# Kernel optimization log

Hardware: AMD Instinct MI355X
Metric: run time of the kernel (lower is better)

The kernel has to match this reference:

```python
import jax, jax.numpy as jnp
import numpy as np

N_HEADS = 16
DIMS = 1024
HEAD_SIZE = DIMS // N_HEADS


def setup_inputs() -> dict:
    key = jax.random.key(0)
    k1, k2, k3, k4, k5 = jax.random.split(key, 5)
    x = jax.random.normal(k1, (1, 4096, DIMS), dtype=jnp.float32)
    s = 1.0 / np.sqrt(DIMS)
    w_qkv = jax.random.uniform(k2, (3 * DIMS, DIMS), jnp.float32, -s, s)
    b_qkv = jax.random.uniform(k3, (3 * DIMS,), jnp.float32, -s, s)
    w_o = jax.random.uniform(k4, (DIMS, DIMS), jnp.float32, -s, s)
    b_o = jax.random.uniform(k5, (DIMS,), jnp.float32, -s, s)
    return {"x": x, "w_qkv": w_qkv, "b_qkv": b_qkv, "w_o": w_o, "b_o": b_o,
            "causal_mask": 1}


def reference(x, w_qkv, b_qkv, w_o, b_o, causal_mask):
    B, S, D = x.shape
    qkv = x @ w_qkv.T + b_qkv                      # [B,S,3D]
    q, k, v = jnp.split(qkv, 3, axis=-1)
    def heads(t):
        return t.reshape(B, S, N_HEADS, HEAD_SIZE).transpose(0, 2, 1, 3)  # [B,H,S,hd]
    q, k, v = heads(q), heads(k), heads(v)
    scores = jnp.einsum("bhsd,bhtd->bhst", q, k)   # [B,H,S,S]
    if causal_mask:
        tri = jnp.triu(jnp.ones((S, S), dtype=bool), k=1)
        scores = jnp.where(tri, -jnp.inf, scores)  # mask BEFORE scale, as in torch code
    scores = scores / np.sqrt(HEAD_SIZE)
    weights = jax.nn.softmax(scores, axis=-1)
    out = jnp.einsum("bhst,bhtd->bhsd", weights, v)  # [B,H,S,hd]
    out = out.transpose(0, 2, 1, 3).reshape(B, S, D)
    return out @ w_o.T + b_o
```

## Files before the change

kernel.cpp:

```cpp
#include <hip/hip_runtime.h>
#include <hip/hip_bf16.h>
#include <stdint.h>

typedef __attribute__((ext_vector_type(8))) short short8;
typedef __attribute__((ext_vector_type(4))) float f32x4;
typedef __attribute__((ext_vector_type(16))) float f32x16;
typedef __attribute__((ext_vector_type(2))) unsigned int uint2u;
typedef __hip_bfloat16 bf16;

#define S_LEN 4096
#define DMODEL 1024
#define NH 16
#define HD 64
#define QSCALE 0.1803368801111f

static __device__ inline uint2 pack4(float4 v) {
  union { uint2 u; bf16 h[4]; } p;
  p.h[0] = (bf16)v.x; p.h[1] = (bf16)v.y; p.h[2] = (bf16)v.z; p.h[3] = (bf16)v.w;
  return p.u;
}

static __device__ inline uint32_t pack2(float a, float b) {
  union { uint32_t u; bf16 h[2]; } p;
  p.h[0] = (bf16)a; p.h[1] = (bf16)b;
  return p.u;
}

static __device__ inline void gload_lds16(const bf16* g, bf16* l) {
  __builtin_amdgcn_global_load_lds(
      (const __attribute__((address_space(1))) unsigned int*)g,
      (__attribute__((address_space(3))) unsigned int*)l, 16, 0, 0);
}

static __device__ inline int rot_idx(int r, int c) {
  return r * 64 + ((c + ((r & 7) << 3)) & 63);
}

__global__ __launch_bounds__(256)
void cvt_all(const float* __restrict__ x, const float* __restrict__ wq,
             const float* __restrict__ wo, bf16* __restrict__ xb,
             bf16* __restrict__ wqb, bf16* __restrict__ wob) {
  const int nx = S_LEN * DMODEL;
  const int nq = 3 * DMODEL * DMODEL;
  const int no = DMODEL * DMODEL;
  int i = (blockIdx.x * 256 + threadIdx.x) * 4;
  if (i < nx) {
    *(uint2*)(xb + i) = pack4(*(const float4*)(x + i));
  } else if (i < nx + nq) {
    int j = i - nx;
    *(uint2*)(wqb + j) = pack4(*(const float4*)(wq + j));
  } else if (i < nx + nq + no) {
    int j = i - nx - nq;
    *(uint2*)(wob + j) = pack4(*(const float4*)(wo + j));
  }
}

__global__ __launch_bounds__(256)
void gemm_qkv(const bf16* __restrict__ A, const bf16* __restrict__ B,
              const float* __restrict__ bias, bf16* __restrict__ qkv2,
              bf16* __restrict__ vt) {
  const int K = DMODEL;
  __shared__ bf16 sA[128 * 64];
  __shared__ bf16 sB[128 * 64];
  const int tid  = threadIdx.x;
  const int lane = tid & 63;
  const int wave = tid >> 6;
  const int wm = wave >> 1, wn = wave & 1;
  const int tileM = blockIdx.y * 128;
  const int tileN = blockIdx.x * 128;

  const int lrow = lane & 15;
  const int quad = lane >> 4;
  const int kq   = quad * 8;

  f32x4 acc[4][4];
#pragma unroll
  for (int i = 0; i < 4; i++)
#pragma unroll
    for (int j = 0; j < 4; j++) acc[i][j] = (f32x4){0.f, 0.f, 0.f, 0.f};

  const int trl = lane >> 3;
  const int cgl = (((lane & 7) - trl) & 7) << 3;
  const bf16* aP[4];
  const bf16* bP[4];
#pragma unroll
  for (int c = 0; c < 4; c++) {
    int ch = wave * 4 + c;
    aP[c] = A + (size_t)(tileM + ch * 8 + trl) * K + cgl;
    bP[c] = B + (size_t)(tileN + ch * 8 + trl) * K + cgl;
  }

  for (int k0 = 0; k0 < K; k0 += 64) {
    __syncthreads();
#pragma unroll
    for (int c = 0; c < 4; c++) {
      int ch = wave * 4 + c;
      gload_lds16(aP[c] + k0, sA + ch * 512);
      gload_lds16(bP[c] + k0, sB + ch * 512);
    }
    __syncthreads();
#pragma unroll
    for (int ks = 0; ks < 2; ks++) {
      short8 afrag[4], bfrag[4];
#pragma unroll
      for (int mi = 0; mi < 4; mi++)
        afrag[mi] = *(const short8*)(sA + rot_idx(wm * 64 + mi * 16 + lrow, ks * 32 + kq));
#pragma unroll
      for (int ni = 0; ni < 4; ni++)
        bfrag[ni] = *(const short8*)(sB + rot_idx(wn * 64 + ni * 16 + lrow, ks * 32 + kq));
#pragma unroll
      for (int mi = 0; mi < 4; mi++)
#pragma unroll
        for (int ni = 0; ni < 4; ni++)
          acc[mi][ni] = __builtin_amdgcn_mfma_f32_16x16x32_bf16(afrag[mi], bfrag[ni], acc[mi][ni], 0, 0, 0);
    }
  }

#pragma unroll
  for (int ni = 0; ni < 4; ni++) {
    int col = tileN + wn * 64 + ni * 16 + lrow;
    float bv = bias[col];
    if (col < 2 * DMODEL) {
      float sc = (col < DMODEL) ? QSCALE : 1.0f;
#pragma unroll
      for (int mi = 0; mi < 4; mi++) {
        int row0 = tileM + wm * 64 + mi * 16 + quad * 4;
#pragma unroll
        for (int r = 0; r < 4; r++)
          qkv2[(size_t)(row0 + r) * 2048 + col] = (bf16)((acc[mi][ni][r] + bv) * sc);
      }
    } else {
      int cc = col - 2 * DMODEL;
      int hh = cc >> 6, dd = cc & 63;
      bf16* vrow = vt + ((size_t)(hh * 64 + dd)) * S_LEN;
#pragma unroll
      for (int mi = 0; mi < 4; mi++) {
        int row0 = tileM + wm * 64 + mi * 16 + quad * 4;
        float4 v = {acc[mi][ni][0] + bv, acc[mi][ni][1] + bv,
                    acc[mi][ni][2] + bv, acc[mi][ni][3] + bv};
        *(uint2*)(vrow + row0) = pack4(v);
      }
    }
  }
}

__global__ __launch_bounds__(256)
void gemm_oproj(const bf16* __restrict__ A, const bf16* __restrict__ B,
                const float* __restrict__ bias, float* __restrict__ C) {
  const int K = DMODEL, N = DMODEL;
  __shared__ bf16 sA[128 * 64];
  __shared__ bf16 sB[64 * 64];
  const int tid  = threadIdx.x;
  const int lane = tid & 63;
  const int wave = tid >> 6;
  const int wm = wave >> 1, wn = wave & 1;
  const int tileM = blockIdx.y * 128;
  const int tileN = blockIdx.x * 64;

  const int lrow = lane & 15;
  const int quad = lane >> 4;
  const int kq   = quad * 8;

  f32x4 acc[4][2];
#pragma unroll
  for (int i = 0; i < 4; i++)
#pragma unroll
    for (int j = 0; j < 2; j++) acc[i][j] = (f32x4){0.f, 0.f, 0.f, 0.f};

  const int trl = lane >> 3;
  const int cgl = (((lane & 7) - trl) & 7) << 3;
  const bf16* aP[4];
  const bf16* bP[2];
#pragma unroll
  for (int c = 0; c < 4; c++) {
    int ch = wave * 4 + c;
    aP[c] = A + (size_t)(tileM + ch * 8 + trl) * K + cgl;
  }
#pragma unroll
  for (int c = 0; c < 2; c++) {
    int ch = wave * 2 + c;
    bP[c] = B + (size_t)(tileN + ch * 8 + trl) * K + cgl;
  }

  for (int k0 = 0; k0 < K; k0 += 64) {
    __syncthreads();
#pragma unroll
    for (int c = 0; c < 4; c++)
      gload_lds16(aP[c] + k0, sA + (wave * 4 + c) * 512);
#pragma unroll
    for (int c = 0; c < 2; c++)
      gload_lds16(bP[c] + k0, sB + (wave * 2 + c) * 512);
    __syncthreads();
#pragma unroll
    for (int ks = 0; ks < 2; ks++) {
      short8 afrag[4], bfrag[2];
#pragma unroll
      for (int mi = 0; mi < 4; mi++)
        afrag[mi] = *(const short8*)(sA + rot_idx(wm * 64 + mi * 16 + lrow, ks * 32 + kq));
#pragma unroll
      for (int ni = 0; ni < 2; ni++)
        bfrag[ni] = *(const short8*)(sB + rot_idx(wn * 32 + ni * 16 + lrow, ks * 32 + kq));
#pragma unroll
      for (int mi = 0; mi < 4; mi++)
#pragma unroll
        for (int ni = 0; ni < 2; ni++)
          acc[mi][ni] = __builtin_amdgcn_mfma_f32_16x16x32_bf16(afrag[mi], bfrag[ni], acc[mi][ni], 0, 0, 0);
    }
  }

#pragma unroll
  for (int ni = 0; ni < 2; ni++) {
    int col = tileN + wn * 32 + ni * 16 + lrow;
    float bv = bias[col];
#pragma unroll
    for (int mi = 0; mi < 4; mi++) {
      int row0 = tileM + wm * 64 + mi * 16 + quad * 4;
#pragma unroll
      for (int r = 0; r < 4; r++)
        C[(size_t)(row0 + r) * N + col] = acc[mi][ni][r] + bv;
    }
  }
}

__global__ __launch_bounds__(256)
void gemm_qkv_f32(const float* __restrict__ A, const float* __restrict__ B,
                  const float* __restrict__ bias, bf16* __restrict__ qkv2,
                  bf16* __restrict__ vt) {
  const int K = DMODEL;
  __shared__ bf16 sA[128 * 64];
  __shared__ bf16 sB[128 * 64];
  const int tid  = threadIdx.x;
  const int lane = tid & 63;
  const int wave = tid >> 6;
  const int wm = wave >> 1, wn = wave & 1;
  const int tileM = blockIdx.y * 128;
  const int tileN = blockIdx.x * 128;
  const int lrow = lane & 15;
  const int quad = lane >> 4;
  const int kq   = quad * 8;

  f32x4 acc[4][4];
#pragma unroll
  for (int i = 0; i < 4; i++)
#pragma unroll
    for (int j = 0; j < 4; j++) acc[i][j] = (f32x4){0.f, 0.f, 0.f, 0.f};

  const int r0 = tid >> 4;
  const int cc = (tid & 15) * 4;

  for (int k0 = 0; k0 < K; k0 += 64) {
    uint2 ra[8], rb[8];
#pragma unroll
    for (int i = 0; i < 8; i++) {
      int row = r0 + i * 16;
      ra[i] = pack4(*(const float4*)(A + (size_t)(tileM + row) * K + k0 + cc));
      rb[i] = pack4(*(const float4*)(B + (size_t)(tileN + row) * K + k0 + cc));
    }
    __syncthreads();
#pragma unroll
    for (int i = 0; i < 8; i++) {
      int row = r0 + i * 16;
      *(uint2*)(sA + row * 64 + cc) = ra[i];
      *(uint2*)(sB + row * 64 + cc) = rb[i];
    }
    __syncthreads();
#pragma unroll
    for (int ks = 0; ks < 2; ks++) {
      short8 afrag[4], bfrag[4];
#pragma unroll
      for (int mi = 0; mi < 4; mi++)
        afrag[mi] = *(const short8*)(sA + (wm * 64 + mi * 16 + lrow) * 64 + ks * 32 + kq);
#pragma unroll
      for (int ni = 0; ni < 4; ni++)
        bfrag[ni] = *(const short8*)(sB + (wn * 64 + ni * 16 + lrow) * 64 + ks * 32 + kq);
#pragma unroll
      for (int mi = 0; mi < 4; mi++)
#pragma unroll
        for (int ni = 0; ni < 4; ni++)
          acc[mi][ni] = __builtin_amdgcn_mfma_f32_16x16x32_bf16(afrag[mi], bfrag[ni], acc[mi][ni], 0, 0, 0);
    }
  }
#pragma unroll
  for (int ni = 0; ni < 4; ni++) {
    int col = tileN + wn * 64 + ni * 16 + lrow;
    float bv = bias[col];
    if (col < 2 * DMODEL) {
      float sc = (col < DMODEL) ? QSCALE : 1.0f;
#pragma unroll
      for (int mi = 0; mi < 4; mi++) {
        int row0 = tileM + wm * 64 + mi * 16 + quad * 4;
#pragma unroll
        for (int r = 0; r < 4; r++)
          qkv2[(size_t)(row0 + r) * 2048 + col] = (bf16)((acc[mi][ni][r] + bv) * sc);
      }
    } else {
      int c2 = col - 2 * DMODEL;
      int hh = c2 >> 6, dd = c2 & 63;
      bf16* vrow = vt + ((size_t)(hh * 64 + dd)) * S_LEN;
#pragma unroll
      for (int mi = 0; mi < 4; mi++) {
        int row0 = tileM + wm * 64 + mi * 16 + quad * 4;
        float4 v = {acc[mi][ni][0] + bv, acc[mi][ni][1] + bv,
                    acc[mi][ni][2] + bv, acc[mi][ni][3] + bv};
        *(uint2*)(vrow + row0) = pack4(v);
      }
    }
  }
}

__global__ __launch_bounds__(256)
void gemm_oproj_f32w(const bf16* __restrict__ A, const float* __restrict__ B,
                     const float* __restrict__ bias, float* __restrict__ C) {
  const int K = DMODEL, N = DMODEL;
  __shared__ bf16 sA[128 * 64];
  __shared__ bf16 sB[128 * 64];
  const int tid  = threadIdx.x;
  const int lane = tid & 63;
  const int wave = tid >> 6;
  const int wm = wave >> 1, wn = wave & 1;
  const int tileM = blockIdx.y * 128;
  const int tileN = blockIdx.x * 128;
  const int lrow = lane & 15;
  const int quad = lane >> 4;
  const int kq   = quad * 8;

  f32x4 acc[4][4];
#pragma unroll
  for (int i = 0; i < 4; i++)
#pragma unroll
    for (int j = 0; j < 4; j++) acc[i][j] = (f32x4){0.f, 0.f, 0.f, 0.f};

  const int a_r0 = tid >> 3;
  const int a_cc = (tid & 7) * 8;
  const int b_r0 = tid >> 4;
  const int b_cc = (tid & 15) * 4;

  for (int k0 = 0; k0 < K; k0 += 64) {
    uint4 ra[4];
    uint2 rb[8];
#pragma unroll
    for (int i = 0; i < 4; i++)
      ra[i] = *(const uint4*)(A + (size_t)(tileM + a_r0 + i * 32) * K + k0 + a_cc);
#pragma unroll
    for (int i = 0; i < 8; i++)
      rb[i] = pack4(*(const float4*)(B + (size_t)(tileN + b_r0 + i * 16) * K + k0 + b_cc));
    __syncthreads();
#pragma unroll
    for (int i = 0; i < 4; i++)
      *(uint4*)(sA + (a_r0 + i * 32) * 64 + a_cc) = ra[i];
#pragma unroll
    for (int i = 0; i < 8; i++)
      *(uint2*)(sB + (b_r0 + i * 16) * 64 + b_cc) = rb[i];
    __syncthreads();
#pragma unroll
    for (int ks = 0; ks < 2; ks++) {
      short8 afrag[4], bfrag[4];
#pragma unroll
      for (int mi = 0; mi < 4; mi++)
        afrag[mi] = *(const short8*)(sA + (wm * 64 + mi * 16 + lrow) * 64 + ks * 32 + kq);
#pragma unroll
      for (int ni = 0; ni < 4; ni++)
        bfrag[ni] = *(const short8*)(sB + (wn * 64 + ni * 16 + lrow) * 64 + ks * 32 + kq);
#pragma unroll
      for (int mi = 0; mi < 4; mi++)
#pragma unroll
        for (int ni = 0; ni < 4; ni++)
          acc[mi][ni] = __builtin_amdgcn_mfma_f32_16x16x32_bf16(afrag[mi], bfrag[ni], acc[mi][ni], 0, 0, 0);
    }
  }
#pragma unroll
  for (int ni = 0; ni < 4; ni++) {
    int col = tileN + wn * 64 + ni * 16 + lrow;
    float bv = bias[col];
#pragma unroll
    for (int mi = 0; mi < 4; mi++) {
      int row0 = tileM + wm * 64 + mi * 16 + quad * 4;
#pragma unroll
      for (int r = 0; r < 4; r++)
        C[(size_t)(row0 + r) * N + col] = acc[mi][ni][r] + bv;
    }
  }
}

__global__ __launch_bounds__(256, 4)
void attn_kernel(const bf16* __restrict__ qkv2, const bf16* __restrict__ vt,
                 bf16* __restrict__ attn_out, const int* __restrict__ causal_ptr) {
  __shared__ bf16 smem[2][64 * 64];
  __shared__ float lbuf[128];

  const int tid  = threadIdx.x;
  const int lane = tid & 63;
  const int wave = tid >> 6;
  const int qh   = wave >> 1;
  const int kh   = wave & 1;

  const int id  = blockIdx.y * 64 + blockIdx.x;
  const int xcd = id & 7;
  const int jj  = id >> 3;
  const int hh  = jj >> 6;
  const int h   = xcd + (hh << 3);
  const int qw  = jj & 63;
  const int qi  = hh ? (63 - qw) : qw;
  const int qbase = qi * 64;
  const bool causal = (*causal_ptr) != 0;

  const int l31 = lane & 31;
  const int hi  = lane >> 5;

  const int trl = lane >> 3;
  const int cgl = (((lane & 7) - trl) & 7) << 3;

  const bf16* Qb = qkv2 + h * HD;
  const bf16* Kb = qkv2 + DMODEL + h * HD;
  const bf16* Vb = vt + (size_t)(h * HD) * S_LEN;

  bf16* const A = smem[0];
  bf16* const B = smem[1];

  const int nkt = causal ? (qi + 1) : (S_LEN / 64);
  const int wrmin = qbase + qh * 32;
  const int wrmax = wrmin + 31;
  const int q_g   = wrmin + l31;

#pragma unroll
  for (int i = 0; i < 2; i++) {
    int ch = wave * 2 + i;
    int trow = ch * 8 + trl;
    gload_lds16(Kb + (size_t)trow * 2048 + cgl, A + ch * 512);
    gload_lds16(Vb + (size_t)trow * S_LEN + cgl, B + ch * 512);
  }
  short8 qf[4];
#pragma unroll
  for (int kd = 0; kd < 4; kd++)
    qf[kd] = *(const short8*)(Qb + (size_t)q_g * 2048 + kd * 16 + hi * 8);

  f32x16 oacc[2];
#pragma unroll
  for (int nc = 0; nc < 2; nc++)
#pragma unroll
    for (int e = 0; e < 16; e++) oacc[nc][e] = 0.f;
  float l_st = 0.f;

  __syncthreads();

  for (int jt = 0; jt < nkt; jt++) {
    const int kbase = jt * 64;
    const int kh32 = kbase + kh * 32;
    const bool live = !(causal && kh32 > wrmax);

    uint32_t pw[2][4];
    if (live) {
      f32x16 sacc;
#pragma unroll
      for (int e = 0; e < 16; e++) sacc[e] = 0.f;
      __builtin_amdgcn_s_setprio(1);
#pragma unroll
      for (int kd = 0; kd < 4; kd++) {
        short8 kf = *(const short8*)(A + rot_idx(kh * 32 + l31, kd * 16 + hi * 8));
        sacc = __builtin_amdgcn_mfma_f32_32x32x16_bf16(kf, qf[kd], sacc, 0, 0, 0);
      }
      __builtin_amdgcn_s_setprio(0);
      const bool nm = causal && (kh32 + 31 > wrmin);
      uint32_t pku[4][2];
      float psum = 0.f;
#pragma unroll
      for (int g = 0; g < 4; g++) {
#pragma unroll
        for (int h2 = 0; h2 < 2; h2++) {
          float v0 = __builtin_amdgcn_exp2f(sacc[g * 4 + h2 * 2]);
          float v1 = __builtin_amdgcn_exp2f(sacc[g * 4 + h2 * 2 + 1]);
          if (nm) {
            int kg = kh32 + g * 8 + hi * 4 + h2 * 2;
            if (kg > q_g)     v0 = 0.f;
            if (kg + 1 > q_g) v1 = 0.f;
          }
          psum += v0 + v1;
          pku[g][h2] = pack2(v0, v1);
        }
      }
      l_st += psum;
#pragma unroll
      for (int c2 = 0; c2 < 2; c2++) {
#pragma unroll
        for (int h2 = 0; h2 < 2; h2++) {
          uint2u sw = __builtin_amdgcn_permlane32_swap(
              pku[2 * c2][h2], pku[2 * c2 + 1][h2], false, false);
          pw[c2][h2]     = sw[0];
          pw[c2][2 + h2] = sw[1];
        }
      }
    }

    __syncthreads();

    if (jt + 1 < nkt) {
      const int kb2 = kbase + 64;
#pragma unroll
      for (int i = 0; i < 2; i++) {
        int ch = wave * 2 + i;
        int trow = ch * 8 + trl;
        gload_lds16(Kb + (size_t)(kb2 + trow) * 2048 + cgl, A + ch * 512);
      }
    }

    if (live) {
      __builtin_amdgcn_s_setprio(1);
#pragma unroll
      for (int c2 = 0; c2 < 2; c2++) {
        if (causal && (kh32 + c2 * 16 > wrmax)) continue;
        union { short8 s; uint32_t u[4]; } pf;
#pragma unroll
        for (int w = 0; w < 4; w++) pf.u[w] = pw[c2][w];
#pragma unroll
        for (int nc = 0; nc < 2; nc++) {
          short8 vf = *(const short8*)(B +
              rot_idx(nc * 32 + l31, (kh * 2 + c2) * 16 + hi * 8));
          oacc[nc] = __builtin_amdgcn_mfma_f32_32x32x16_bf16(pf.s, vf, oacc[nc], 0, 0, 0);
        }
      }
      __builtin_amdgcn_s_setprio(0);
    }

    __syncthreads();

    if (jt + 1 < nkt) {
      const int kb2 = kbase + 64;
#pragma unroll
      for (int i = 0; i < 2; i++) {
        int ch = wave * 2 + i;
        int trow = ch * 8 + trl;
        gload_lds16(Vb + (size_t)trow * S_LEN + kb2 + cgl, B + ch * 512);
      }
    }
  }

  float ltot = l_st + __shfl_xor(l_st, 32);
  float* obuf = (float*)smem;
  if (kh == 1) {
    float* ob = obuf + qh * 2048;
#pragma unroll
    for (int nc = 0; nc < 2; nc++)
#pragma unroll
      for (int e = 0; e < 16; e++)
        ob[(nc * 16 + e) * 64 + lane] = oacc[nc][e];
    if (hi == 0) lbuf[qh * 32 + l31] = ltot;
  }
  __syncthreads();
  if (kh == 0) {
    float* ob = obuf + qh * 2048;
#pragma unroll
    for (int nc = 0; nc < 2; nc++)
#pragma unroll
      for (int e = 0; e < 16; e++)
        oacc[nc][e] += ob[(nc * 16 + e) * 64 + lane];
    ltot += lbuf[qh * 32 + l31];
    if (hi == 0) lbuf[64 + qh * 32 + l31] = ltot;
    float invl[4][4];
#pragma unroll
    for (int g = 0; g < 4; g++) {
      f32x4 lv = *(const f32x4*)(lbuf + 64 + qh * 32 + g * 8 + hi * 4);
#pragma unroll
      for (int r = 0; r < 4; r++) invl[g][r] = 1.0f / fmaxf(lv[r], 1e-30f);
    }
#pragma unroll
    for (int nc = 0; nc < 2; nc++) {
#pragma unroll
      for (int g = 0; g < 4; g++) {
#pragma unroll
        for (int r = 0; r < 4; r++) {
          int qg = qbase + qh * 32 + g * 8 + hi * 4 + r;
          int col = h * HD + nc * 32 + l31;
          attn_out[(size_t)qg * DMODEL + col] = (bf16)(oacc[nc][g * 4 + r] * invl[g][r]);
        }
      }
    }
  }
}

extern "C" void kernel_launch(void* const* d_in, const int* in_sizes, int n_in,
                              void* d_out, int out_size, void* d_ws, size_t ws_size,
                              hipStream_t stream) {
  const float* x     = (const float*)d_in[0];
  const float* w_qkv = (const float*)d_in[1];
  const float* b_qkv = (const float*)d_in[2];
  const float* w_o   = (const float*)d_in[3];
  const float* b_o   = (const float*)d_in[4];
  const int*   cm    = (const int*)d_in[5];

  char* ws = (char*)d_ws;
  bf16* qkv2 = (bf16*)ws;
  bf16* vt   = (bf16*)(ws + 16777216);
  bf16* attn = (bf16*)(ws + 25165824);
  bf16* xb   = (bf16*)(ws + 33554432);
  bf16* wqb  = (bf16*)(ws + 41943040);
  bf16* wob  = (bf16*)(ws + 48234496);

  dim3 blk(256);
  const bool fast = (ws_size >= (size_t)50331648);

  if (fast) {
    const int ntot = S_LEN * DMODEL + 3 * DMODEL * DMODEL + DMODEL * DMODEL;
    cvt_all<<<dim3((ntot / 4 + 255) / 256), blk, 0, stream>>>(
        x, w_qkv, w_o, xb, wqb, wob);
    gemm_qkv<<<dim3(3 * DMODEL / 128, S_LEN / 128), blk, 0, stream>>>(
        xb, wqb, b_qkv, qkv2, vt);
    attn_kernel<<<dim3(S_LEN / 64, NH), blk, 0, stream>>>(qkv2, vt, attn, cm);
    gemm_oproj<<<dim3(DMODEL / 64, S_LEN / 128), blk, 0, stream>>>(
        attn, wob, b_o, (float*)d_out);
  } else {
    gemm_qkv_f32<<<dim3(3 * DMODEL / 128, S_LEN / 128), blk, 0, stream>>>(
        x, w_qkv, b_qkv, qkv2, vt);
    attn_kernel<<<dim3(S_LEN / 64, NH), blk, 0, stream>>>(qkv2, vt, attn, cm);
    gemm_oproj_f32w<<<dim3(DMODEL / 128, S_LEN / 128), blk, 0, stream>>>(
        attn, w_o, b_o, (float*)d_out);
  }
}
```

Baseline: 219.3 us.

## Restructure attention blocks: 32-query tiles with 4-way key split and paired causal tiles

Each attention block now handles two 32-row query tiles, one from each end of the causal triangle, so per-block work is balanced. All four waves share the same 32 queries and split each 128-key step four ways, then reduce partial outputs and row sums through shared memory. The grid shrinks to 1024 blocks and each block loads 128 keys per iteration into a shared buffer twice as large. This targets causal load imbalance and idle waves on the diagonal. The cost is a 4-way cross-wave reduction per tile and extra synchronisation, with more LDS per block that may lower occupancy.

Measured after the change: 232.8 us. 1.06x slower.

```diff
diff --git a/kernel.cpp b/kernel.cpp
--- a/kernel.cpp
+++ b/kernel.cpp
@@ -385,28 +385,24 @@
 __global__ __launch_bounds__(256, 4)
 void attn_kernel(const bf16* __restrict__ qkv2, const bf16* __restrict__ vt,
                  bf16* __restrict__ attn_out, const int* __restrict__ causal_ptr) {
-  __shared__ bf16 smem[2][64 * 64];
+  __shared__ bf16 smem[2][128 * 64];
   __shared__ float lbuf[128];
 
   const int tid  = threadIdx.x;
   const int lane = tid & 63;
   const int wave = tid >> 6;
-  const int qh   = wave >> 1;
+  const int p    = wave >> 1;
   const int kh   = wave & 1;
 
   const int id  = blockIdx.y * 64 + blockIdx.x;
   const int xcd = id & 7;
-  const int jj  = id >> 3;
-  const int hh  = jj >> 6;
+  const int hh  = (id >> 3) & 1;
+  const int idx = id >> 4;
   const int h   = xcd + (hh << 3);
-  const int qw  = jj & 63;
-  const int qi  = hh ? (63 - qw) : qw;
-  const int qbase = qi * 64;
   const bool causal = (*causal_ptr) != 0;
 
   const int l31 = lane & 31;
   const int hi  = lane >> 5;
-
   const int trl = lane >> 3;
   const int cgl = (((lane & 7) - trl) & 7) << 3;
 
@@ -414,163 +410,176 @@
   const bf16* Kb = qkv2 + DMODEL + h * HD;
   const bf16* Vb = vt + (size_t)(h * HD) * S_LEN;
 
-  bf16* const A = smem[0];
-  bf16* const B = smem[1];
-
-  const int nkt = causal ? (qi + 1) : (S_LEN / 64);
-  const int wrmin = qbase + qh * 32;
-  const int wrmax = wrmin + 31;
-  const int q_g   = wrmin + l31;
-
-#pragma unroll
-  for (int i = 0; i < 2; i++) {
-    int ch = wave * 2 + i;
-    int trow = ch * 8 + trl;
-    gload_lds16(Kb + (size_t)trow * 2048 + cgl, A + ch * 512);
-    gload_lds16(Vb + (size_t)trow * S_LEN + cgl, B + ch * 512);
-  }
-  short8 qf[4];
-#pragma unroll
-  for (int kd = 0; kd < 4; kd++)
-    qf[kd] = *(const short8*)(Qb + (size_t)q_g * 2048 + kd * 16 + hi * 8);
-
-  f32x16 oacc[2];
-#pragma unroll
-  for (int nc = 0; nc < 2; nc++)
-#pragma unroll
-    for (int e = 0; e < 16; e++) oacc[nc][e] = 0.f;
-  float l_st = 0.f;
-
-  __syncthreads();
-
-  for (int jt = 0; jt < nkt; jt++) {
-    const int kbase = jt * 64;
-    const int kh32 = kbase + kh * 32;
-    const bool live = !(causal && kh32 > wrmax);
-
-    uint32_t pw[2][4];
-    if (live) {
-      f32x16 sacc;
-#pragma unroll
-      for (int e = 0; e < 16; e++) sacc[e] = 0.f;
-      __builtin_amdgcn_s_setprio(1);
-#pragma unroll
-      for (int kd = 0; kd < 4; kd++) {
-        short8 kf = *(const short8*)(A + rot_idx(kh * 32 + l31, kd * 16 + hi * 8));
-        sacc = __builtin_amdgcn_mfma_f32_32x32x16_bf16(kf, qf[kd], sacc, 0, 0, 0);
-      }
-      __builtin_amdgcn_s_setprio(0);
-      const bool nm = causal && (kh32 + 31 > wrmin);
-      uint32_t pku[4][2];
-      float psum = 0.f;
+  bf16* const A  = smem[0];
+  bf16* const B0 = smem[1];
+  bf16* const B1 = smem[1] + 4096;
+  const bf16* const Ap = smem[0] + p * 4096;
+  const bf16* const Bp = smem[1] + p * 4096;
+
+  const bf16* const kB = Kb + (size_t)(wave * 32 + trl) * 2048 + cgl;
+  const bf16* const vB = Vb + (size_t)(wave * 16 + trl) * S_LEN + cgl;
+
+  for (int a = 0; a < 2; a++) {
+    const int qi    = a ? (127 - idx) : idx;
+    const int qbase = qi * 32;
+    const int q_g   = qbase + l31;
+    const int wrmax = qbase + 31;
+    const int niter = causal ? ((qi >> 2) + 1) : 32;
+
+    __syncthreads();
+
+#pragma unroll
+    for (int i = 0; i < 4; i++)
+      gload_lds16(kB + (size_t)i * 8 * 2048, A + (wave * 4 + i) * 512);
+#pragma unroll
+    for (int i = 0; i < 2; i++) {
+      gload_lds16(vB + (size_t)i * 8 * S_LEN,      B0 + (wave * 2 + i) * 512);
+      gload_lds16(vB + (size_t)i * 8 * S_LEN + 64, B1 + (wave * 2 + i) * 512);
+    }
+    short8 qf[4];
+#pragma unroll
+    for (int kd = 0; kd < 4; kd++)
+      qf[kd] = *(const short8*)(Qb + (size_t)q_g * 2048 + kd * 16 + hi * 8);
+
+    f32x16 oacc[2];
+#pragma unroll
+    for (int nc = 0; nc < 2; nc++)
+#pragma unroll
+      for (int e = 0; e < 16; e++) oacc[nc][e] = 0.f;
+    float l_st = 0.f;
+
+    const bf16* kP = kB + (size_t)128 * 2048;
+    const bf16* vP = vB + 128;
+
+    __syncthreads();
+
+    for (int jt = 0; jt < niter; jt++) {
+      const int kh32 = jt * 128 + p * 64 + kh * 32;
+      const bool live = !(causal && kh32 > wrmax);
+
+      uint32_t pw[2][4];
+      if (live) {
+        f32x16 sacc;
+#pragma unroll
+        for (int e = 0; e < 16; e++) sacc[e] = 0.f;
+        __builtin_amdgcn_s_setprio(1);
+#pragma unroll
+        for (int kd = 0; kd < 4; kd++) {
+          short8 kf = *(const short8*)(Ap + rot_idx(kh * 32 + l31, kd * 16 + hi * 8));
+          sacc = __builtin_amdgcn_mfma_f32_32x32x16_bf16(kf, qf[kd], sacc, 0, 0, 0);
+        }
+        __builtin_amdgcn_s_setprio(0);
+        const bool nm = causal && (kh32 + 31 > qbase);
+        uint32_t pku[4][2];
+        float psum = 0.f;
+#pragma unroll
+        for (int g = 0; g < 4; g++) {
+#pragma unroll
+          for (int h2 = 0; h2 < 2; h2++) {
+            float v0 = __builtin_amdgcn_exp2f(sacc[g * 4 + h2 * 2]);
+            float v1 = __builtin_amdgcn_exp2f(sacc[g * 4 + h2 * 2 + 1]);
+            if (nm) {
+              int kg = kh32 + g * 8 + hi * 4 + h2 * 2;
+              if (kg > q_g)     v0 = 0.f;
+              if (kg + 1 > q_g) v1 = 0.f;
+            }
+            psum += v0 + v1;
+            pku[g][h2] = pack2(v0, v1);
+          }
+        }
+        l_st += psum;
+#pragma unroll
+        for (int c2 = 0; c2 < 2; c2++) {
+#pragma unroll
+          for (int h2 = 0; h2 < 2; h2++) {
+            uint2u sw = __builtin_amdgcn_permlane32_swap(
+                pku[2 * c2][h2], pku[2 * c2 + 1][h2], false, false);
+            pw[c2][h2]     = sw[0];
+            pw[c2][2 + h2] = sw[1];
+          }
+        }
+      }
+
+      __syncthreads();
+
+      if (jt + 1 < niter) {
+#pragma unroll
+        for (int i = 0; i < 4; i++)
+          gload_lds16(kP + (size_t)i * 8 * 2048, A + (wave * 4 + i) * 512);
+        kP += (size_t)128 * 2048;
+      }
+
+      if (live) {
+        __builtin_amdgcn_s_setprio(1);
+#pragma unroll
+        for (int c2 = 0; c2 < 2; c2++) {
+          if (causal && (kh32 + c2 * 16 > wrmax)) continue;
+          union { short8 s; uint32_t u[4]; } pf;
+#pragma unroll
+          for (int w = 0; w < 4; w++) pf.u[w] = pw[c2][w];
+#pragma unroll
+          for (int nc = 0; nc < 2; nc++) {
+            short8 vf = *(const short8*)(Bp +
+                rot_idx(nc * 32 + l31, (kh * 2 + c2) * 16 + hi * 8));
+            oacc[nc] = __builtin_amdgcn_mfma_f32_32x32x16_bf16(pf.s, vf, oacc[nc], 0, 0, 0);
+          }
+        }
+        __builtin_amdgcn_s_setprio(0);
+      }
+
+      __syncthreads();
+
+      if (jt + 1 < niter) {
+#pragma unroll
+        for (int i = 0; i < 2; i++) {
+          gload_lds16(vP + (size_t)i * 8 * S_LEN,      B0 + (wave * 2 + i) * 512);
+          gload_lds16(vP + (size_t)i * 8 * S_LEN + 64, B1 + (wave * 2 + i) * 512);
+        }
+        vP += 128;
+      }
+    }
+
+    float ltot = l_st + __shfl_xor(l_st, 32);
+    float* obuf = (float*)smem;
+    if (wave != 0) {
+      float* ob = obuf + (wave - 1) * 2048;
+#pragma unroll
+      for (int nc = 0; nc < 2; nc++)
+#pragma unroll
+        for (int e = 0; e < 16; e++)
+          ob[(nc * 16 + e) * 64 + lane] = oacc[nc][e];
+      if (hi == 0) lbuf[wave * 32 + l31] = ltot;
+    }
+    __syncthreads();
+    if (wave == 0) {
+#pragma unroll
+      for (int w = 0; w < 3; w++) {
+        float* ob = obuf + w * 2048;
+#pragma unroll
+        for (int nc = 0; nc < 2; nc++)
+#pragma unroll
+          for (int e = 0; e < 16; e++)
+            oacc[nc][e] += ob[(nc * 16 + e) * 64 + lane];
+      }
+      ltot += lbuf[32 + l31] + lbuf[64 + l31] + lbuf[96 + l31];
+      if (hi == 0) lbuf[l31] = ltot;
+      float invl[4][4];
 #pragma unroll
       for (int g = 0; g < 4; g++) {
-#pragma unroll
-        for (int h2 = 0; h2 < 2; h2++) {
-          float v0 = __builtin_amdgcn_exp2f(sacc[g * 4 + h2 * 2]);
-          float v1 = __builtin_amdgcn_exp2f(sacc[g * 4 + h2 * 2 + 1]);
-          if (nm) {
-            int kg = kh32 + g * 8 + hi * 4 + h2 * 2;
-            if (kg > q_g)     v0 = 0.f;
-            if (kg + 1 > q_g) v1 = 0.f;
+        f32x4 lv = *(const f32x4*)(lbuf + g * 8 + hi * 4);
+#pragma unroll
+        for (int r = 0; r < 4; r++) invl[g][r] = 1.0f / fmaxf(lv[r], 1e-30f);
+      }
+#pragma unroll
+      for (int nc = 0; nc < 2; nc++) {
+#pragma unroll
+        for (int g = 0; g < 4; g++) {
+#pragma unroll
+          for (int r = 0; r < 4; r++) {
+            int qg = qbase + g * 8 + hi * 4 + r;
+            int col = h * HD + nc * 32 + l31;
+            attn_out[(size_t)qg * DMODEL + col] = (bf16)(oacc[nc][g * 4 + r] * invl[g][r]);
           }
-          psum += v0 + v1;
-          pku[g][h2] = pack2(v0, v1);
-        }
-      }
-      l_st += psum;
-#pragma unroll
-      for (int c2 = 0; c2 < 2; c2++) {
-#pragma unroll
-        for (int h2 = 0; h2 < 2; h2++) {
-          uint2u sw = __builtin_amdgcn_permlane32_swap(
-              pku[2 * c2][h2], pku[2 * c2 + 1][h2], false, false);
-          pw[c2][h2]     = sw[0];
-          pw[c2][2 + h2] = sw[1];
-        }
-      }
-    }
-
-    __syncthreads();
-
-    if (jt + 1 < nkt) {
-      const int kb2 = kbase + 64;
-#pragma unroll
-      for (int i = 0; i < 2; i++) {
-        int ch = wave * 2 + i;
-        int trow = ch * 8 + trl;
-        gload_lds16(Kb + (size_t)(kb2 + trow) * 2048 + cgl, A + ch * 512);
-      }
-    }
-
-    if (live) {
-      __builtin_amdgcn_s_setprio(1);
-#pragma unroll
-      for (int c2 = 0; c2 < 2; c2++) {
-        if (causal && (kh32 + c2 * 16 > wrmax)) continue;
-        union { short8 s; uint32_t u[4]; } pf;
-#pragma unroll
-        for (int w = 0; w < 4; w++) pf.u[w] = pw[c2][w];
-#pragma unroll
-        for (int nc = 0; nc < 2; nc++) {
-          short8 vf = *(const short8*)(B +
-              rot_idx(nc * 32 + l31, (kh * 2 + c2) * 16 + hi * 8));
-          oacc[nc] = __builtin_amdgcn_mfma_f32_32x32x16_bf16(pf.s, vf, oacc[nc], 0, 0, 0);
-        }
-      }
-      __builtin_amdgcn_s_setprio(0);
-    }
-
-    __syncthreads();
-
-    if (jt + 1 < nkt) {
-      const int kb2 = kbase + 64;
-#pragma unroll
-      for (int i = 0; i < 2; i++) {
-        int ch = wave * 2 + i;
-        int trow = ch * 8 + trl;
-        gload_lds16(Vb + (size_t)trow * S_LEN + kb2 + cgl, B + ch * 512);
-      }
-    }
-  }
-
-  float ltot = l_st + __shfl_xor(l_st, 32);
-  float* obuf = (float*)smem;
-  if (kh == 1) {
-    float* ob = obuf + qh * 2048;
-#pragma unroll
-    for (int nc = 0; nc < 2; nc++)
-#pragma unroll
-      for (int e = 0; e < 16; e++)
-        ob[(nc * 16 + e) * 64 + lane] = oacc[nc][e];
-    if (hi == 0) lbuf[qh * 32 + l31] = ltot;
-  }
-  __syncthreads();
-  if (kh == 0) {
-    float* ob = obuf + qh * 2048;
-#pragma unroll
-    for (int nc = 0; nc < 2; nc++)
-#pragma unroll
-      for (int e = 0; e < 16; e++)
-        oacc[nc][e] += ob[(nc * 16 + e) * 64 + lane];
-    ltot += lbuf[qh * 32 + l31];
-    if (hi == 0) lbuf[64 + qh * 32 + l31] = ltot;
-    float invl[4][4];
-#pragma unroll
-    for (int g = 0; g < 4; g++) {
-      f32x4 lv = *(const f32x4*)(lbuf + 64 + qh * 32 + g * 8 + hi * 4);
-#pragma unroll
-      for (int r = 0; r < 4; r++) invl[g][r] = 1.0f / fmaxf(lv[r], 1e-30f);
-    }
-#pragma unroll
-    for (int nc = 0; nc < 2; nc++) {
-#pragma unroll
-      for (int g = 0; g < 4; g++) {
-#pragma unroll
-        for (int r = 0; r < 4; r++) {
-          int qg = qbase + qh * 32 + g * 8 + hi * 4 + r;
-          int col = h * HD + nc * 32 + l31;
-          attn_out[(size_t)qg * DMODEL + col] = (bf16)(oacc[nc][g * 4 + r] * invl[g][r]);
         }
       }
     }
@@ -604,13 +613,13 @@
         x, w_qkv, w_o, xb, wqb, wob);
     gemm_qkv<<<dim3(3 * DMODEL / 128, S_LEN / 128), blk, 0, stream>>>(
         xb, wqb, b_qkv, qkv2, vt);
-    attn_kernel<<<dim3(S_LEN / 64, NH), blk, 0, stream>>>(qkv2, vt, attn, cm);
+    attn_kernel<<<dim3(64, NH), blk, 0, stream>>>(qkv2, vt, attn, cm);
     gemm_oproj<<<dim3(DMODEL / 64, S_LEN / 128), blk, 0, stream>>>(
         attn, wob, b_o, (float*)d_out);
   } else {
     gemm_qkv_f32<<<dim3(3 * DMODEL / 128, S_LEN / 128), blk, 0, stream>>>(
         x, w_qkv, b_qkv, qkv2, vt);
-    attn_kernel<<<dim3(S_LEN / 64, NH), blk, 0, stream>>>(qkv2, vt, attn, cm);
+    attn_kernel<<<dim3(64, NH), blk, 0, stream>>>(qkv2, vt, attn, cm);
     gemm_oproj_f32w<<<dim3(DMODEL / 128, S_LEN / 128), blk, 0, stream>>>(
         attn, w_o, b_o, (float*)d_out);
   }
```

## Split attention KV range into two halves with separate merge kernel

Applied to the files above, without the earlier changes.

Each query tile's key range is split across two blocks (split-K), doubling the attention grid and scheduling the longest causal tiles first. Partial unnormalized outputs go to bf16 scratch buffers placed in the output buffer, and row sums are stashed in the attention output rows. A new merge kernel adds the two partials and normalizes. This targets causal load imbalance and tail effects, at the cost of an extra launch, extra global traffic, and bf16 rounding of the partial sums.

Result: faster. 205.2 us (-6.4%).

```diff
diff --git a/kernel.cpp b/kernel.cpp
--- a/kernel.cpp
+++ b/kernel.cpp
@@ -24,6 +24,10 @@
   union { uint32_t u; bf16 h[2]; } p;
   p.h[0] = (bf16)a; p.h[1] = (bf16)b;
   return p.u;
+}
+
+static __device__ inline float b2f(short s) {
+  union { short s; bf16 h; } u; u.s = s; return (float)u.h;
 }
 
 static __device__ inline void gload_lds16(const bf16* g, bf16* l) {
@@ -384,9 +388,10 @@
 
 __global__ __launch_bounds__(256, 4)
 void attn_kernel(const bf16* __restrict__ qkv2, const bf16* __restrict__ vt,
-                 bf16* __restrict__ attn_out, const int* __restrict__ causal_ptr) {
+                 bf16* __restrict__ attn_out, const int* __restrict__ causal_ptr,
+                 bf16* __restrict__ p0, bf16* __restrict__ p1) {
   __shared__ bf16 smem[2][64 * 64];
-  __shared__ float lbuf[128];
+  __shared__ float lbuf[64];
 
   const int tid  = threadIdx.x;
   const int lane = tid & 63;
@@ -394,19 +399,18 @@
   const int qh   = wave >> 1;
   const int kh   = wave & 1;
 
-  const int id  = blockIdx.y * 64 + blockIdx.x;
-  const int xcd = id & 7;
-  const int jj  = id >> 3;
-  const int hh  = jj >> 6;
-  const int h   = xcd + (hh << 3);
-  const int qw  = jj & 63;
-  const int qi  = hh ? (63 - qw) : qw;
+  const int id   = blockIdx.y * 128 + blockIdx.x;
+  const int xcd  = id & 7;
+  const int hh   = (id >> 3) & 1;
+  const int h    = xcd + (hh << 3);
+  const int ck   = (id >> 4) & 1;
+  const int rank = id >> 5;
+  const int qi   = 63 - rank;
   const int qbase = qi * 64;
   const bool causal = (*causal_ptr) != 0;
 
   const int l31 = lane & 31;
   const int hi  = lane >> 5;
-
   const int trl = lane >> 3;
   const int cgl = (((lane & 7) - trl) & 7) << 3;
 
@@ -417,17 +421,23 @@
   bf16* const A = smem[0];
   bf16* const B = smem[1];
 
-  const int nkt = causal ? (qi + 1) : (S_LEN / 64);
+  const int Lt   = causal ? (qi + 1) : (S_LEN / 64);
+  const int half = (Lt + 1) >> 1;
+  const int jt0  = ck ? half : 0;
+  const int jt1  = ck ? Lt : half;
+
   const int wrmin = qbase + qh * 32;
   const int wrmax = wrmin + 31;
   const int q_g   = wrmin + l31;
 
-#pragma unroll
-  for (int i = 0; i < 2; i++) {
-    int ch = wave * 2 + i;
-    int trow = ch * 8 + trl;
-    gload_lds16(Kb + (size_t)trow * 2048 + cgl, A + ch * 512);
-    gload_lds16(Vb + (size_t)trow * S_LEN + cgl, B + ch * 512);
+  if (jt0 < jt1) {
+#pragma unroll
+    for (int i = 0; i < 2; i++) {
+      int ch = wave * 2 + i;
+      int trow = ch * 8 + trl;
+      gload_lds16(Kb + (size_t)(jt0 * 64 + trow) * 2048 + cgl, A + ch * 512);
+      gload_lds16(Vb + (size_t)trow * S_LEN + jt0 * 64 + cgl, B + ch * 512);
+    }
   }
   short8 qf[4];
 #pragma unroll
@@ -443,7 +453,7 @@
 
   __syncthreads();
 
-  for (int jt = 0; jt < nkt; jt++) {
+  for (int jt = jt0; jt < jt1; jt++) {
     const int kbase = jt * 64;
     const int kh32 = kbase + kh * 32;
     const bool live = !(causal && kh32 > wrmax);
@@ -493,7 +503,7 @@
 
     __syncthreads();
 
-    if (jt + 1 < nkt) {
+    if (jt + 1 < jt1) {
       const int kb2 = kbase + 64;
 #pragma unroll
       for (int i = 0; i < 2; i++) {
@@ -523,7 +533,7 @@
 
     __syncthreads();
 
-    if (jt + 1 < nkt) {
+    if (jt + 1 < jt1) {
       const int kb2 = kbase + 64;
 #pragma unroll
       for (int i = 0; i < 2; i++) {
@@ -554,27 +564,66 @@
       for (int e = 0; e < 16; e++)
         oacc[nc][e] += ob[(nc * 16 + e) * 64 + lane];
     ltot += lbuf[qh * 32 + l31];
-    if (hi == 0) lbuf[64 + qh * 32 + l31] = ltot;
-    float invl[4][4];
-#pragma unroll
-    for (int g = 0; g < 4; g++) {
-      f32x4 lv = *(const f32x4*)(lbuf + 64 + qh * 32 + g * 8 + hi * 4);
-#pragma unroll
-      for (int r = 0; r < 4; r++) invl[g][r] = 1.0f / fmaxf(lv[r], 1e-30f);
-    }
-#pragma unroll
-    for (int nc = 0; nc < 2; nc++) {
-#pragma unroll
-      for (int g = 0; g < 4; g++) {
-#pragma unroll
-        for (int r = 0; r < 4; r++) {
-          int qg = qbase + qh * 32 + g * 8 + hi * 4 + r;
-          int col = h * HD + nc * 32 + l31;
-          attn_out[(size_t)qg * DMODEL + col] = (bf16)(oacc[nc][g * 4 + r] * invl[g][r]);
-        }
-      }
-    }
-  }
+
+    if (hi == 0) {
+      float* lrow = (float*)(attn_out +
+          (size_t)(qbase + ck * 2 + qh) * DMODEL + h * HD);
+      lrow[l31] = ltot;
+    }
+    bf16* po = (ck ? p1 : p0) + (size_t)(h * 64 + qi) * 4096;
+#pragma unroll
+    for (int nc = 0; nc < 2; nc++)
+#pragma unroll
+      for (int g = 0; g < 4; g++)
+#pragma unroll
+        for (int r = 0; r < 4; r++)
+          po[(qh * 32 + g * 8 + hi * 4 + r) * 64 + nc * 32 + l31] =
+              (bf16)oacc[nc][g * 4 + r];
+  }
+}
+
+__global__ __launch_bounds__(256)
+void attn_merge(const bf16* __restrict__ p0, const bf16* __restrict__ p1,
+                bf16* __restrict__ attn_out) {
+  const int qi = blockIdx.x;
+  const int h  = blockIdx.y;
+  const int tid = threadIdx.x;
+  const int qbase = qi * 64;
+  __shared__ float lsh[128];
+  if (tid < 128) {
+    int ckv  = tid >> 6;
+    int qhv  = (tid >> 5) & 1;
+    int l31v = tid & 31;
+    const float* lrow = (const float*)(attn_out +
+        (size_t)(qbase + ckv * 2 + qhv) * DMODEL + h * HD);
+    lsh[ckv * 64 + qhv * 32 + l31v] = lrow[l31v];
+  }
+  __syncthreads();
+
+  const int q  = tid >> 2;
+  const int d0 = (tid & 3) * 16;
+  const float linv = 1.0f / fmaxf(lsh[q] + lsh[64 + q], 1e-30f);
+  const size_t slot = (size_t)(h * 64 + qi) * 4096 + q * 64 + d0;
+  short8 x0 = *(const short8*)(p0 + slot);
+  short8 x1 = *(const short8*)(p0 + slot + 8);
+  short8 y0 = *(const short8*)(p1 + slot);
+  short8 y1 = *(const short8*)(p1 + slot + 8);
+  uint32_t w[8];
+#pragma unroll
+  for (int j = 0; j < 4; j++) {
+    float a = (b2f(x0[2 * j])     + b2f(y0[2 * j]))     * linv;
+    float b = (b2f(x0[2 * j + 1]) + b2f(y0[2 * j + 1])) * linv;
+    w[j] = pack2(a, b);
+  }
+#pragma unroll
+  for (int j = 0; j < 4; j++) {
+    float a = (b2f(x1[2 * j])     + b2f(y1[2 * j]))     * linv;
+    float b = (b2f(x1[2 * j + 1]) + b2f(y1[2 * j + 1])) * linv;
+    w[4 + j] = pack2(a, b);
+  }
+  bf16* outp = attn_out + (size_t)(qbase + q) * DMODEL + h * HD + d0;
+  *(uint4*)(outp)     = (uint4){w[0], w[1], w[2], w[3]};
+  *(uint4*)(outp + 8) = (uint4){w[4], w[5], w[6], w[7]};
 }
 
 extern "C" void kernel_launch(void* const* d_in, const int* in_sizes, int n_in,
@@ -595,6 +644,9 @@
   bf16* wqb  = (bf16*)(ws + 41943040);
   bf16* wob  = (bf16*)(ws + 48234496);
 
+  bf16* p0 = (bf16*)d_out;
+  bf16* p1 = (bf16*)d_out + 4194304;
+
   dim3 blk(256);
   const bool fast = (ws_size >= (size_t)50331648);
 
@@ -604,13 +656,15 @@
         x, w_qkv, w_o, xb, wqb, wob);
     gemm_qkv<<<dim3(3 * DMODEL / 128, S_LEN / 128), blk, 0, stream>>>(
         xb, wqb, b_qkv, qkv2, vt);
-    attn_kernel<<<dim3(S_LEN / 64, NH), blk, 0, stream>>>(qkv2, vt, attn, cm);
+    attn_kernel<<<dim3(128, NH), blk, 0, stream>>>(qkv2, vt, attn, cm, p0, p1);
+    attn_merge<<<dim3(64, NH), blk, 0, stream>>>(p0, p1, attn);
     gemm_oproj<<<dim3(DMODEL / 64, S_LEN / 128), blk, 0, stream>>>(
         attn, wob, b_o, (float*)d_out);
   } else {
     gemm_qkv_f32<<<dim3(3 * DMODEL / 128, S_LEN / 128), blk, 0, stream>>>(
         x, w_qkv, b_qkv, qkv2, vt);
-    attn_kernel<<<dim3(S_LEN / 64, NH), blk, 0, stream>>>(qkv2, vt, attn, cm);
+    attn_kernel<<<dim3(128, NH), blk, 0, stream>>>(qkv2, vt, attn, cm, p0, p1);
+    attn_merge<<<dim3(64, NH), blk, 0, stream>>>(p0, p1, attn);
     gemm_oproj_f32w<<<dim3(DMODEL / 128, S_LEN / 128), blk, 0, stream>>>(
         attn, w_o, b_o, (float*)d_out);
   }
```
